# Kernel tuning notes

Measured on AMD Instinct MI355X. Metric: run time of the kernel, lower is better.

## Reference

```python
import jax, jax.numpy as jnp
import numpy as np

HIDDEN = 3584
N_HEADS = 28
N_KV = 4
HEAD_DIM = HIDDEN // N_HEADS  # 128
BS, SEQ = 4, 2048
EPS = 1e-6
ROPE_THETA = 1000000.0


def setup_inputs() -> dict:
    key = jax.random.key(0)
    ks = jax.random.split(key, 9)
    s = 0.02
    x = jax.random.normal(ks[0], (BS, SEQ, HIDDEN), dtype=jnp.float32)
    positions = jnp.broadcast_to(jnp.arange(SEQ, dtype=jnp.int32), (BS, SEQ))
    ln_w = jnp.ones((HIDDEN,), dtype=jnp.float32)
    Wq = jax.random.normal(ks[1], (N_HEADS * HEAD_DIM, HIDDEN), dtype=jnp.float32) * s
    bq = jax.random.normal(ks[2], (N_HEADS * HEAD_DIM,), dtype=jnp.float32) * s
    Wk = jax.random.normal(ks[3], (N_KV * HEAD_DIM, HIDDEN), dtype=jnp.float32) * s
    bk = jax.random.normal(ks[4], (N_KV * HEAD_DIM,), dtype=jnp.float32) * s
    Wv = jax.random.normal(ks[5], (N_KV * HEAD_DIM, HIDDEN), dtype=jnp.float32) * s
    bv = jax.random.normal(ks[6], (N_KV * HEAD_DIM,), dtype=jnp.float32) * s
    Wo = jax.random.normal(ks[7], (HIDDEN, N_HEADS * HEAD_DIM), dtype=jnp.float32) * s
    return {"x": x, "positions": positions, "ln_w": ln_w, "Wq": Wq, "bq": bq,
            "Wk": Wk, "bk": bk, "Wv": Wv, "bv": bv, "Wo": Wo}


def _rms_norm(x, w, eps):
    var = jnp.mean(x * x, axis=-1, keepdims=True)
    return x * jax.lax.rsqrt(var + eps) * w


def _rope(x, positions):
    # x: [b, s, h, d], neox-style rotary, theta = ROPE_THETA
    d = x.shape[-1]
    inv_freq = 1.0 / (ROPE_THETA ** (jnp.arange(0, d, 2, dtype=jnp.float32) / d))
    ang = positions.astype(jnp.float32)[..., None] * inv_freq  # [b, s, d/2]
    cos = jnp.cos(ang)[:, :, None, :]
    sin = jnp.sin(ang)[:, :, None, :]
    x1, x2 = jnp.split(x, 2, axis=-1)
    return jnp.concatenate([x1 * cos - x2 * sin, x2 * cos + x1 * sin], axis=-1)


def reference(x, positions, ln_w, Wq, bq, Wk, bk, Wv, bv, Wo):
    bs, seq, _ = x.shape
    h = _rms_norm(x, ln_w, EPS)
    q = jnp.einsum('bsh,oh->bso', h, Wq) + bq
    k = jnp.einsum('bsh,oh->bso', h, Wk) + bk
    v = jnp.einsum('bsh,oh->bso', h, Wv) + bv  # computed but unused downstream (as in source)
    q = _rope(q.reshape(bs, seq, N_HEADS, HEAD_DIM), positions)
    k = _rope(k.reshape(bs, seq, N_KV, HEAD_DIM), positions)  # unused downstream (as in source)
    out = jnp.einsum('bso,ho->bsh', q.reshape(bs, seq, -1), Wo) + x
    return out
```

## Files before the change

### kernel.cpp

```cpp
#include <hip/hip_runtime.h>
#include <hip/hip_bf16.h>


#define HIDDEN   3584
#define NQ       3584
#define NTOK     8192
#define NPAIR    64
#define EPSV     1e-6f

typedef __hip_bfloat16 bf16;
typedef __bf16 bf16x8 __attribute__((ext_vector_type(8)));
typedef float  f32x4  __attribute__((ext_vector_type(4)));

static __device__ __forceinline__ unsigned short f2bu(float f) {
  bf16 h = __float2bfloat16(f);
  return __builtin_bit_cast(unsigned short, h);
}
static __device__ __forceinline__ void stv(float* p, float v) { *p = v; }
static __device__ __forceinline__ void stv(bf16* p, float v) { *p = __float2bfloat16(v); }

__global__ __launch_bounds__(256)
void cvt_f32_bf16(const float* __restrict__ s, bf16* __restrict__ d, int n4) {
  int i = blockIdx.x * 256 + threadIdx.x;
  if (i >= n4) return;
  float4 f = ((const float4*)s)[i];
  ushort4 o;
  o.x = f2bu(f.x); o.y = f2bu(f.y); o.z = f2bu(f.z); o.w = f2bu(f.w);
  ((ushort4*)d)[i] = o;
}

__global__ __launch_bounds__(256)
void rmsnorm_k(const float* __restrict__ x, const float* __restrict__ w,
               bf16* __restrict__ h) {
  const int row = blockIdx.x;
  const int t = threadIdx.x;
  const float4* xr = (const float4*)(x + (size_t)row * HIDDEN);
  const float4* wr = (const float4*)w;

  float4 v0 = xr[t], v1 = xr[t + 256], v2 = xr[t + 512];
  float4 v3 = make_float4(0.f, 0.f, 0.f, 0.f);
  if (t < 128) v3 = xr[t + 768];

  float ss = v0.x*v0.x + v0.y*v0.y + v0.z*v0.z + v0.w*v0.w
           + v1.x*v1.x + v1.y*v1.y + v1.z*v1.z + v1.w*v1.w
           + v2.x*v2.x + v2.y*v2.y + v2.z*v2.z + v2.w*v2.w
           + v3.x*v3.x + v3.y*v3.y + v3.z*v3.z + v3.w*v3.w;

#pragma unroll
  for (int off = 32; off > 0; off >>= 1) ss += __shfl_down(ss, off);
  __shared__ float red[4];
  if ((t & 63) == 0) red[t >> 6] = ss;
  __syncthreads();
  float tot = red[0] + red[1] + red[2] + red[3];
  float scale = rsqrtf(tot * (1.0f / HIDDEN) + EPSV);

  ushort4* hr = (ushort4*)(h + (size_t)row * HIDDEN);
  float4 w0 = wr[t], w1 = wr[t + 256], w2 = wr[t + 512];
  ushort4 o;
  o.x = f2bu(v0.x*scale*w0.x); o.y = f2bu(v0.y*scale*w0.y);
  o.z = f2bu(v0.z*scale*w0.z); o.w = f2bu(v0.w*scale*w0.w);
  hr[t] = o;
  o.x = f2bu(v1.x*scale*w1.x); o.y = f2bu(v1.y*scale*w1.y);
  o.z = f2bu(v1.z*scale*w1.z); o.w = f2bu(v1.w*scale*w1.w);
  hr[t + 256] = o;
  o.x = f2bu(v2.x*scale*w2.x); o.y = f2bu(v2.y*scale*w2.y);
  o.z = f2bu(v2.z*scale*w2.z); o.w = f2bu(v2.w*scale*w2.w);
  hr[t + 512] = o;
  if (t < 128) {
    float4 w3 = wr[t + 768];
    o.x = f2bu(v3.x*scale*w3.x); o.y = f2bu(v3.y*scale*w3.y);
    o.z = f2bu(v3.z*scale*w3.z); o.w = f2bu(v3.w*scale*w3.w);
    hr[t + 768] = o;
  }
}

__global__ __launch_bounds__(256)
void rope_tab_k(const int* __restrict__ pos, float2* __restrict__ tab) {
  int idx = blockIdx.x * 256 + threadIdx.x;
  int t = idx >> 6;
  int i = idx & 63;
  float inv = exp2f(-(float)i * (19.931568569324174f / 64.0f));
  float ang = (float)pos[t] * inv;
  float s, c;
  sincosf(ang, &s, &c);
  tab[idx] = make_float2(c, s);
}

__global__ __launch_bounds__(256)
void rope_apply_k(bf16* __restrict__ q, const float2* __restrict__ tab) {
  const int t = blockIdx.x;
  bf16* qt = q + (size_t)t * NQ;
  const float2* tb = tab + (size_t)t * NPAIR;
  for (int j = threadIdx.x; j < 28 * NPAIR; j += 256) {
    int head = j >> 6;
    int i = j & 63;
    float2 cs = tb[i];
    int base = head * 128 + i;
    float x1 = __bfloat162float(qt[base]);
    float x2 = __bfloat162float(qt[base + 64]);
    qt[base]      = __float2bfloat16(x1 * cs.x - x2 * cs.y);
    qt[base + 64] = __float2bfloat16(x2 * cs.x + x1 * cs.y);
  }
}

#define BMT 256
#define BNT 256
#define BKT 64

#define FENCE() asm volatile("" ::: "memory")
#define BAR() do { FENCE(); __builtin_amdgcn_s_barrier(); FENCE(); } while (0)
#define VMW(n) asm volatile("s_waitcnt vmcnt(" #n ")" ::: "memory")

template <int MODE, typename OutT>
__global__ __launch_bounds__(512, 2)
void gemm256(const bf16* __restrict__ A, const bf16* __restrict__ B,
             const float* __restrict__ aux, OutT* __restrict__ C,
             int M, int N, int K) {
  __shared__ __align__(16) bf16 sA[2][BMT][BKT];
  __shared__ __align__(16) bf16 sB[2][BNT][BKT];

  const int tid  = threadIdx.x;
  const int wave = tid >> 6;
  const int lane = tid & 63;
  const int wm   = wave >> 2;
  const int wn   = wave & 3;
  const int fr   = lane & 15;
  const int ks   = lane >> 4;
  const int sx   = fr & 7;

  const int nwg = gridDim.x;
  const int cpx = nwg >> 3;
  const int swz = (blockIdx.x & 7) * cpx + (blockIdx.x >> 3);
  const int gn  = N / BNT;
  const int bm  = (swz / gn) * BMT;
  const int bn  = (swz % gn) * BNT;

  const bf16* Ab = A + (size_t)bm * K;
  const bf16* Bb = B + (size_t)bn * K;

  const int NT = K / BKT;

  const int srw = lane >> 3;
  const int ssl = lane & 7;

  auto stage64 = [&](const bf16* gpanel, int kt, bf16* ldst, int rbase) {
    const int r  = rbase + wave * 8 + srw;
    const int sg = ssl ^ srw;
    const bf16* src = gpanel + (size_t)r * K + (size_t)kt * BKT + sg * 8;
    __builtin_amdgcn_global_load_lds(
        (const __attribute__((address_space(1))) void*)src,
        (__attribute__((address_space(3))) void*)(ldst + (size_t)(wave * 8) * BKT),
        16, 0, 0);
  };
  auto stage16k = [&](int kind, int buf, int kt) {
    if (kt >= NT) return;
    if (kind == 0)      { stage64(Ab, kt, &sA[buf][0][0],   0);   stage64(Ab, kt, &sA[buf][128][0], 128); }
    else if (kind == 1) { stage64(Ab, kt, &sA[buf][64][0],  64);  stage64(Ab, kt, &sA[buf][192][0], 192); }
    else if (kind == 2) { stage64(Bb, kt, &sB[buf][0][0],   0);   stage64(Bb, kt, &sB[buf][64][0],  64); }
    else                { stage64(Bb, kt, &sB[buf][128][0], 128); stage64(Bb, kt, &sB[buf][192][0], 192); }
  };

  f32x4 acc[8][4];
#pragma unroll
  for (int i = 0; i < 8; ++i)
#pragma unroll
    for (int j = 0; j < 4; ++j)
      acc[i][j] = (f32x4){0.f, 0.f, 0.f, 0.f};

  stage16k(2, 0, 0); stage16k(3, 0, 0); stage16k(0, 0, 0); stage16k(1, 0, 0);
  stage16k(2, 1, 1); stage16k(3, 1, 1); stage16k(0, 1, 1);
  VMW(6);
  BAR();

  bf16x8 bfr[4][2];
  const int nit = NT / 2;

  for (int it = 0; it < nit; ++it) {
    const bool last = (it == nit - 1);
#pragma unroll
    for (int u = 0; u < 2; ++u) {
#pragma unroll
      for (int q = 0; q < 4; ++q) {
        bf16x8 afr[2][2];
#pragma unroll
        for (int i = 0; i < 2; ++i)
#pragma unroll
          for (int kk = 0; kk < 2; ++kk) {
            const int R  = wm * 128 + q * 32 + i * 16 + fr;
            const int sp = (kk * 4 + ks) ^ sx;
            afr[i][kk] = *(const bf16x8*)&sA[u][R][sp * 8];
          }
        if (q == 0) {
#pragma unroll
          for (int j = 0; j < 4; ++j)
#pragma unroll
            for (int kk = 0; kk < 2; ++kk) {
              const int R  = wn * 64 + j * 16 + fr;
              const int sp = (kk * 4 + ks) ^ sx;
              bfr[j][kk] = *(const bf16x8*)&sB[u][R][sp * 8];
            }
        }
        const int ph = u * 4 + q;
        if (ph == 0)      stage16k(1, 1, 2 * it + 1);
        else if (ph == 1) stage16k(2, 0, 2 * it + 2);
        else if (ph == 2) stage16k(3, 0, 2 * it + 2);
        else if (ph == 3) stage16k(0, 0, 2 * it + 2);
        else if (ph == 4) stage16k(1, 0, 2 * it + 2);
        else if (ph == 5) stage16k(2, 1, 2 * it + 3);
        else if (ph == 6) stage16k(3, 1, 2 * it + 3);
        else              stage16k(0, 1, 2 * it + 3);
        if (q == 0) asm volatile("s_waitcnt lgkmcnt(8)" ::: "memory");
        BAR();
        asm volatile("s_waitcnt lgkmcnt(0)" ::: "memory");
        __builtin_amdgcn_sched_barrier(0);
        __builtin_amdgcn_s_setprio(1);
#pragma unroll
        for (int i = 0; i < 2; ++i)
#pragma unroll
          for (int j = 0; j < 4; ++j)
#pragma unroll
            for (int kk = 0; kk < 2; ++kk)
              acc[q * 2 + i][j] = __builtin_amdgcn_mfma_f32_16x16x32_bf16(
                  afr[i][kk], bfr[j][kk], acc[q * 2 + i][j], 0, 0, 0);
        __builtin_amdgcn_s_setprio(0);
        if (q == 1) {
          if (!last) VMW(10);
          else if (u == 0) VMW(8);
          else VMW(0);
        } else if (q == 3) {
          if (!last) VMW(8);
          else if (u == 0) VMW(2);
          else VMW(0);
        }
        BAR();
      }
    }
  }

#pragma unroll
  for (int f = 0; f < 8; ++f) {
    const int rb = bm + wm * 128 + f * 16 + ks * 4;
#pragma unroll
    for (int j = 0; j < 4; ++j) {
      const int col = bn + wn * 64 + j * 16 + fr;
#pragma unroll
      for (int r = 0; r < 4; ++r) {
        const int row = rb + r;
        float v = acc[f][j][r];
        if (MODE == 0) v += aux[col];
        else           v += aux[(size_t)row * N + col];
        stv(&C[(size_t)row * N + col], v);
      }
    }
  }
}

extern "C" void kernel_launch(void* const* d_in, const int* in_sizes, int n_in,
                              void* d_out, int out_size, void* d_ws, size_t ws_size,
                              hipStream_t stream) {
  (void)in_sizes; (void)n_in; (void)out_size; (void)ws_size;
  const float* x    = (const float*)d_in[0];
  const int*   pos  = (const int*)d_in[1];
  const float* ln_w = (const float*)d_in[2];
  const float* Wq   = (const float*)d_in[3];
  const float* bq   = (const float*)d_in[4];
  const float* Wo   = (const float*)d_in[9];
  float* out = (float*)d_out;

  char* ws = (char*)d_ws;
  size_t off = 0;
  bf16* h    = (bf16*)(ws + off); off += (size_t)NTOK * HIDDEN * sizeof(bf16);
  bf16* q    = (bf16*)(ws + off); off += (size_t)NTOK * NQ * sizeof(bf16);
  bf16* Wqb  = (bf16*)(ws + off); off += (size_t)NQ * HIDDEN * sizeof(bf16);
  bf16* Wob  = (bf16*)(ws + off); off += (size_t)HIDDEN * NQ * sizeof(bf16);
  float2* tab = (float2*)(ws + off); off += (size_t)NTOK * NPAIR * sizeof(float2);

  const int n4 = NQ * HIDDEN / 4;
  cvt_f32_bf16<<<(n4 + 255) / 256, 256, 0, stream>>>(Wq, Wqb, n4);
  cvt_f32_bf16<<<(n4 + 255) / 256, 256, 0, stream>>>(Wo, Wob, n4);
  rmsnorm_k<<<NTOK, 256, 0, stream>>>(x, ln_w, h);
  rope_tab_k<<<(NTOK * NPAIR) / 256, 256, 0, stream>>>(pos, tab);

  const int nblk = (NTOK / BMT) * (NQ / BNT);
  gemm256<0, bf16><<<nblk, 512, 0, stream>>>(h, Wqb, bq, q, NTOK, NQ, HIDDEN);
  rope_apply_k<<<NTOK, 256, 0, stream>>>(q, tab);
  gemm256<1, float><<<nblk, 512, 0, stream>>>(q, Wob, x, out, NTOK, HIDDEN, NQ);
}
```

Measured before the change: 501.1 us.

## Double-buffer A fragments in registers to overlap LDS reads with MFMA

Splits the A-fragment LDS reads into two register sets (afrP/afrQ) so the next quarter's A fragment is loaded while the current quarter's MFMAs run, using partial lgkmcnt waits instead of waiting for all reads. It also moves the vmcnt waits for staged global loads (q==1 becomes q==0, last-iteration waits changed). The aim is to hide LDS latency behind matrix math. The cost is extra VGPRs under launch bounds of 512 threads with 2 blocks, which risks spills, and the new wait counts could be wrong and race with the async buffer loads.

```diff
diff --git a/kernel.cpp b/kernel.cpp
--- a/kernel.cpp
+++ b/kernel.cpp
@@ -109,7 +109,8 @@
 
 #define FENCE() asm volatile("" ::: "memory")
 #define BAR() do { FENCE(); __builtin_amdgcn_s_barrier(); FENCE(); } while (0)
-#define VMW(n) asm volatile("s_waitcnt vmcnt(" #n ")" ::: "memory")
+#define VMW(n)  asm volatile("s_waitcnt vmcnt(" #n ")" ::: "memory")
+#define LGKM(n) asm volatile("s_waitcnt lgkmcnt(" #n ")" ::: "memory")
 
 template <int MODE, typename OutT>
 __global__ __launch_bounds__(512, 2)
@@ -167,12 +168,46 @@
     for (int j = 0; j < 4; ++j)
       acc[i][j] = (f32x4){0.f, 0.f, 0.f, 0.f};
 
+  bf16x8 bfr[4][2];
+  bf16x8 afrP[2][2];
+  bf16x8 afrQ[2][2];
+
+  auto loadA = [&](int buf, int qq, bf16x8 (&dst)[2][2]) {
+#pragma unroll
+    for (int i = 0; i < 2; ++i)
+#pragma unroll
+      for (int kk = 0; kk < 2; ++kk) {
+        const int R  = wm * 128 + qq * 32 + i * 16 + fr;
+        const int sp = (kk * 4 + ks) ^ sx;
+        dst[i][kk] = *(const bf16x8*)&sA[buf][R][sp * 8];
+      }
+  };
+  auto loadB = [&](int buf) {
+#pragma unroll
+    for (int j = 0; j < 4; ++j)
+#pragma unroll
+      for (int kk = 0; kk < 2; ++kk) {
+        const int R  = wn * 64 + j * 16 + fr;
+        const int sp = (kk * 4 + ks) ^ sx;
+        bfr[j][kk] = *(const bf16x8*)&sB[buf][R][sp * 8];
+      }
+  };
+  auto domfma = [&](int q, bf16x8 (&af)[2][2]) {
+#pragma unroll
+    for (int i = 0; i < 2; ++i)
+#pragma unroll
+      for (int j = 0; j < 4; ++j)
+#pragma unroll
+        for (int kk = 0; kk < 2; ++kk)
+          acc[q * 2 + i][j] = __builtin_amdgcn_mfma_f32_16x16x32_bf16(
+              af[i][kk], bfr[j][kk], acc[q * 2 + i][j], 0, 0, 0);
+  };
+
   stage16k(2, 0, 0); stage16k(3, 0, 0); stage16k(0, 0, 0); stage16k(1, 0, 0);
   stage16k(2, 1, 1); stage16k(3, 1, 1); stage16k(0, 1, 1);
   VMW(6);
   BAR();
 
-  bf16x8 bfr[4][2];
   const int nit = NT / 2;
 
   for (int it = 0; it < nit; ++it) {
@@ -181,26 +216,17 @@
     for (int u = 0; u < 2; ++u) {
 #pragma unroll
       for (int q = 0; q < 4; ++q) {
-        bf16x8 afr[2][2];
-#pragma unroll
-        for (int i = 0; i < 2; ++i)
-#pragma unroll
-          for (int kk = 0; kk < 2; ++kk) {
-            const int R  = wm * 128 + q * 32 + i * 16 + fr;
-            const int sp = (kk * 4 + ks) ^ sx;
-            afr[i][kk] = *(const bf16x8*)&sA[u][R][sp * 8];
-          }
+        const int ph = u * 4 + q;
         if (q == 0) {
-#pragma unroll
-          for (int j = 0; j < 4; ++j)
-#pragma unroll
-            for (int kk = 0; kk < 2; ++kk) {
-              const int R  = wn * 64 + j * 16 + fr;
-              const int sp = (kk * 4 + ks) ^ sx;
-              bfr[j][kk] = *(const bf16x8*)&sB[u][R][sp * 8];
-            }
+          loadA(u, 0, afrP);
+          loadB(u);
+          __builtin_amdgcn_sched_barrier(0);
+          loadA(u, 1, afrQ);
+        } else if (q == 1) {
+          loadA(u, 2, afrP);
+        } else if (q == 2) {
+          loadA(u, 3, afrQ);
         }
-        const int ph = u * 4 + q;
         if (ph == 0)      stage16k(1, 1, 2 * it + 1);
         else if (ph == 1) stage16k(2, 0, 2 * it + 2);
         else if (ph == 2) stage16k(3, 0, 2 * it + 2);
@@ -209,28 +235,21 @@
         else if (ph == 5) stage16k(2, 1, 2 * it + 3);
         else if (ph == 6) stage16k(3, 1, 2 * it + 3);
         else              stage16k(0, 1, 2 * it + 3);
-        if (q == 0) asm volatile("s_waitcnt lgkmcnt(8)" ::: "memory");
         BAR();
-        asm volatile("s_waitcnt lgkmcnt(0)" ::: "memory");
+        if (q < 3) LGKM(4);
+        else       LGKM(0);
         __builtin_amdgcn_sched_barrier(0);
         __builtin_amdgcn_s_setprio(1);
-#pragma unroll
-        for (int i = 0; i < 2; ++i)
-#pragma unroll
-          for (int j = 0; j < 4; ++j)
-#pragma unroll
-            for (int kk = 0; kk < 2; ++kk)
-              acc[q * 2 + i][j] = __builtin_amdgcn_mfma_f32_16x16x32_bf16(
-                  afr[i][kk], bfr[j][kk], acc[q * 2 + i][j], 0, 0, 0);
+        if ((q & 1) == 0) domfma(q, afrP);
+        else              domfma(q, afrQ);
         __builtin_amdgcn_s_setprio(0);
-        if (q == 1) {
-          if (!last) VMW(10);
-          else if (u == 0) VMW(8);
-          else VMW(0);
+        if (q == 0) {
+          if (!last)       { VMW(8); }
+          else if (u == 0) { VMW(8); }
+          else             { VMW(0); }
         } else if (q == 3) {
-          if (!last) VMW(8);
-          else if (u == 0) VMW(2);
-          else VMW(0);
+          if (!last)       { VMW(8); }
+          else if (u == 0) { VMW(2); }
         }
         BAR();
       }
```

New measurement: 504.5 us. No clear change (+0.7%).
